# Kernel optimization log

Measured on AMD Instinct MI355X. Metric: run time of the kernel, lower is better.

Reference implementation:

```python
import jax, jax.numpy as jnp
import numpy as np
import math

H = 16
D_MODEL = 1024
D_K = 64
BS = 8
SEQ = 1024


def setup_inputs() -> dict:
    key = jax.random.key(0)
    ks = jax.random.split(key, 13)
    s = 1.0 / math.sqrt(D_MODEL)
    inp = {
        "q": jax.random.normal(ks[0], (BS, SEQ, D_MODEL), dtype=jnp.float32),
        "k": jax.random.normal(ks[1], (BS, SEQ, D_MODEL), dtype=jnp.float32),
        "v": jax.random.normal(ks[2], (BS, SEQ, D_MODEL), dtype=jnp.float32),
        "mask": jax.random.randint(ks[3], (BS, SEQ, SEQ), 0, 2, dtype=jnp.int32),
        "Wq": jax.random.normal(ks[4], (D_MODEL, D_MODEL), dtype=jnp.float32) * s,
        "bq": jax.random.normal(ks[5], (D_MODEL,), dtype=jnp.float32) * s,
        "Wk": jax.random.normal(ks[6], (D_MODEL, D_MODEL), dtype=jnp.float32) * s,
        "bk": jax.random.normal(ks[7], (D_MODEL,), dtype=jnp.float32) * s,
        "Wv": jax.random.normal(ks[8], (D_MODEL, D_MODEL), dtype=jnp.float32) * s,
        "bv": jax.random.normal(ks[9], (D_MODEL,), dtype=jnp.float32) * s,
        "Wo": jax.random.normal(ks[10], (D_MODEL, D_MODEL), dtype=jnp.float32) * s,
        "bo": jax.random.normal(ks[11], (D_MODEL,), dtype=jnp.float32) * s,
    }
    return inp


def reference(q, k, v, mask, Wq, bq, Wk, bk, Wv, bv, Wo, bo):
    bs, seq, _ = q.shape
    # projections, split heads: [b, h, s, dk]
    def proj(x, W, b):
        y = x @ W + b
        return y.reshape(bs, seq, H, D_K).transpose(0, 2, 1, 3)
    qh = proj(q, Wq, bq)
    kh = proj(k, Wk, bk)
    vh = proj(v, Wv, bv)
    # scaled dot-product attention (dropout is identity in eval mode)
    scores = jnp.einsum("bhqd,bhkd->bhqk", qh, kh) / math.sqrt(D_K)
    scores = jnp.where(mask[:, None, :, :] == 0, jnp.float32(-1e9), scores)
    attn = jax.nn.softmax(scores, axis=-1)
    ctx = jnp.einsum("bhqk,bhkd->bhqd", attn, vh)
    concat = ctx.transpose(0, 2, 1, 3).reshape(bs, seq, D_MODEL)
    return concat @ Wo + bo
```

## Files before the change

kernel.cpp:

```cpp
#include <hip/hip_runtime.h>
#include <hip/hip_bf16.h>

#define HN 16
#define DM 1024
#define DK 64
#define BSZ 8
#define SEQL 1024

typedef __attribute__((ext_vector_type(8))) short bf16x8;
typedef __attribute__((ext_vector_type(4))) short short4v;
typedef __attribute__((ext_vector_type(4))) float f32x4;

__device__ __forceinline__ short f2bf(float f) {
    union { float f; unsigned u; } x; x.f = f;
    unsigned u = x.u + 0x7FFFu + ((x.u >> 16) & 1u);
    return (short)(u >> 16);
}

__device__ __forceinline__ void async16(const short* g, short* ldsbase) {
    __builtin_amdgcn_global_load_lds(
        (const __attribute__((address_space(1))) unsigned int*)g,
        (__attribute__((address_space(3))) unsigned int*)ldsbase, 16, 0, 0);
}

__global__ __launch_bounds__(256) void cast_bf16(const float* __restrict__ in,
                                                 short* __restrict__ out) {
    size_t i = (size_t)blockIdx.x * 256 + threadIdx.x;
    float4 a = ((const float4*)in)[2 * i];
    float4 b = ((const float4*)in)[2 * i + 1];
    bf16x8 r = {f2bf(a.x), f2bf(a.y), f2bf(a.z), f2bf(a.w),
                f2bf(b.x), f2bf(b.y), f2bf(b.z), f2bf(b.w)};
    ((bf16x8*)out)[i] = r;
}

__global__ __launch_bounds__(256) void transpose_cast(const float* __restrict__ W,
                                                      short* __restrict__ Wt) {
    __shared__ float tile[32][33];
    const int t = threadIdx.x;
    const int k0 = blockIdx.x * 32, n0 = blockIdx.y * 32;
    const int c = t & 31, r = t >> 5;
    #pragma unroll
    for (int p = 0; p < 4; ++p)
        tile[r + 8 * p][c] = W[(size_t)(k0 + r + 8 * p) * DM + n0 + c];
    __syncthreads();
    #pragma unroll
    for (int p = 0; p < 4; ++p)
        Wt[(size_t)(n0 + r + 8 * p) * DM + k0 + c] = f2bf(tile[c][r + 8 * p]);
}

__global__ __launch_bounds__(256) void pack_mask(const int* __restrict__ mask,
                                                 unsigned long long* __restrict__ bits) {
    size_t i = (size_t)blockIdx.x * 256 + threadIdx.x;
    unsigned long long b = __ballot(mask[i] != 0);
    if ((threadIdx.x & 63) == 0) bits[i >> 6] = b;
}

template <int MODE>
__global__ __launch_bounds__(256) void gemm_mfma(const short* __restrict__ A,
                                                 const short* __restrict__ Wt,
                                                 const float* __restrict__ bias,
                                                 void* __restrict__ Cp) {
    __shared__ __attribute__((aligned(16))) short As[128][32];
    __shared__ __attribute__((aligned(16))) short Bs[128][32];
    const int t = threadIdx.x;
    const int lane = t & 63, wv = t >> 6;
    const int wm = (wv >> 1) * 64, wn = (wv & 1) * 64;
    const int quad = lane >> 4, l15 = lane & 15;
    const int tileM = blockIdx.x * 128, tileN = blockIdx.y * 128;
    const size_t zoff = (size_t)blockIdx.z * DM * SEQL;
    const short* Az = A + zoff;

    const int sr = wv * 16 + (lane >> 2);
    const int sc = (lane & 3) * 8;

    f32x4 acc[4][4];
    #pragma unroll
    for (int i = 0; i < 4; ++i)
        #pragma unroll
        for (int j = 0; j < 4; ++j) acc[i][j] = {0.f, 0.f, 0.f, 0.f};

    for (int k0 = 0; k0 < DM; k0 += 32) {
        #pragma unroll
        for (int p = 0; p < 2; ++p) {
            async16(Az + (size_t)(tileM + p * 64 + sr) * DM + k0 + sc,
                    &As[p * 64 + wv * 16][0]);
            async16(Wt + (size_t)(tileN + p * 64 + sr) * DM + k0 + sc,
                    &Bs[p * 64 + wv * 16][0]);
        }
        __syncthreads();
        bf16x8 a[4], b[4];
        #pragma unroll
        for (int i = 0; i < 4; ++i) a[i] = *(const bf16x8*)&As[wm + i * 16 + l15][quad * 8];
        #pragma unroll
        for (int j = 0; j < 4; ++j) b[j] = *(const bf16x8*)&Bs[wn + j * 16 + l15][quad * 8];
        #pragma unroll
        for (int i = 0; i < 4; ++i)
            #pragma unroll
            for (int j = 0; j < 4; ++j)
                acc[i][j] = __builtin_amdgcn_mfma_f32_16x16x32_bf16(a[i], b[j], acc[i][j], 0, 0, 0);
        __syncthreads();
    }

    #pragma unroll
    for (int i = 0; i < 4; ++i)
        #pragma unroll
        for (int j = 0; j < 4; ++j)
            #pragma unroll
            for (int rr = 0; rr < 4; ++rr) {
                int row = tileM + wm + i * 16 + quad * 4 + rr;
                int col = tileN + wn + j * 16 + l15;
                float v = acc[i][j][rr] + bias[col];
                if (MODE == 0) {
                    short* C = (short*)Cp + zoff;
                    C[((size_t)(col >> 6) * SEQL + row) * DK + (col & 63)] = f2bf(v);
                } else if (MODE == 1) {
                    float* C = (float*)Cp + zoff;
                    C[(size_t)row * DM + col] = v;
                } else {
                    short* C = (short*)Cp + zoff;
                    C[(size_t)col * SEQL + row] = f2bf(v);
                }
            }
}

template <bool USE_BITS>
__global__ __launch_bounds__(256) void attn_mfma(const short* __restrict__ Qw,
                                                 const short* __restrict__ Kw,
                                                 const short* __restrict__ Vt,
                                                 const void* __restrict__ maskp,
                                                 short* __restrict__ ctx) {
    __shared__ __attribute__((aligned(16))) short Qs[64][72];
    __shared__ __attribute__((aligned(16))) short Ks[64][72];
    __shared__ __attribute__((aligned(16))) short Vs[64][72];
    __shared__ __attribute__((aligned(16))) short Ps[4][16][72];
    const int t = threadIdx.x;
    const int lane = t & 63, w = t >> 6;
    const int quad = lane >> 4, l15 = lane & 15;
    const int q0 = blockIdx.x * 64;
    const int h = blockIdx.y;
    const size_t zoff = (size_t)blockIdx.z * DM * SEQL;
    const short* Qb = Qw + zoff + (size_t)h * SEQL * DK;
    const short* Kb = Kw + zoff + (size_t)h * SEQL * DK;
    const short* Vb = Vt + zoff + (size_t)h * DK * SEQL;

    #pragma unroll
    for (int p = 0; p < 2; ++p) {
        int cc = t + 256 * p;
        int row = cc >> 3, off = (cc & 7) * 8;
        *(bf16x8*)&Qs[row][off] = *(const bf16x8*)(Qb + (size_t)(q0 + row) * DK + off);
    }

    f32x4 o[4];
    #pragma unroll
    for (int td = 0; td < 4; ++td) o[td] = {0.f, 0.f, 0.f, 0.f};
    float Lacc[4] = {0.f, 0.f, 0.f, 0.f};

    for (int j0 = 0; j0 < SEQL; j0 += 64) {
        #pragma unroll
        for (int p = 0; p < 2; ++p) {
            int cc = t + 256 * p;
            int row = cc >> 3, off = (cc & 7) * 8;
            *(bf16x8*)&Ks[row][off] = *(const bf16x8*)(Kb + (size_t)(j0 + row) * DK + off);
            *(bf16x8*)&Vs[row][off] = *(const bf16x8*)(Vb + (size_t)row * SEQL + j0 + off);
        }
        __syncthreads();

        unsigned long long mw[4];
        if (USE_BITS) {
            const unsigned long long* mb =
                (const unsigned long long*)maskp + (size_t)blockIdx.z * SEQL * 16;
            #pragma unroll
            for (int rr = 0; rr < 4; ++rr)
                mw[rr] = mb[(size_t)(q0 + w * 16 + quad * 4 + rr) * 16 + (j0 >> 6)];
        }

        #pragma unroll
        for (int tn = 0; tn < 4; ++tn) {
            f32x4 s = {0.f, 0.f, 0.f, 0.f};
            #pragma unroll
            for (int ks = 0; ks < 2; ++ks) {
                bf16x8 aq = *(const bf16x8*)&Qs[w * 16 + l15][ks * 32 + quad * 8];
                bf16x8 bk = *(const bf16x8*)&Ks[tn * 16 + l15][ks * 32 + quad * 8];
                s = __builtin_amdgcn_mfma_f32_16x16x32_bf16(aq, bk, s, 0, 0, 0);
            }
            #pragma unroll
            for (int rr = 0; rr < 4; ++rr) {
                bool keep;
                if (USE_BITS) {
                    keep = (mw[rr] >> (tn * 16 + l15)) & 1ull;
                } else {
                    const int* mb = (const int*)maskp + (size_t)blockIdx.z * SEQL * SEQL;
                    keep = mb[(size_t)(q0 + w * 16 + quad * 4 + rr) * SEQL + j0 + tn * 16 + l15] != 0;
                }
                float p = keep ? __expf(s[rr] * 0.125f) : 0.0f;
                Lacc[rr] += p;
                Ps[w][quad * 4 + rr][tn * 16 + l15] = f2bf(p);
            }
        }
        #pragma unroll
        for (int td = 0; td < 4; ++td)
            #pragma unroll
            for (int ks = 0; ks < 2; ++ks) {
                bf16x8 ap = *(const bf16x8*)&Ps[w][l15][ks * 32 + quad * 8];
                bf16x8 bv = *(const bf16x8*)&Vs[td * 16 + l15][ks * 32 + quad * 8];
                o[td] = __builtin_amdgcn_mfma_f32_16x16x32_bf16(ap, bv, o[td], 0, 0, 0);
            }
        __syncthreads();
    }

    #pragma unroll
    for (int rr = 0; rr < 4; ++rr) {
        float l = Lacc[rr];
        l += __shfl_xor(l, 1);
        l += __shfl_xor(l, 2);
        l += __shfl_xor(l, 4);
        l += __shfl_xor(l, 8);
        Lacc[rr] = 1.0f / l;
    }
    short* cb = ctx + zoff;
    #pragma unroll
    for (int td = 0; td < 4; ++td)
        #pragma unroll
        for (int rr = 0; rr < 4; ++rr) {
            int rq = q0 + w * 16 + quad * 4 + rr;
            int cd = h * 64 + td * 16 + l15;
            cb[(size_t)rq * DM + cd] = f2bf(o[td][rr] * Lacc[rr]);
        }
}

extern "C" void kernel_launch(void* const* d_in, const int* in_sizes, int n_in,
                              void* d_out, int out_size, void* d_ws, size_t ws_size,
                              hipStream_t stream) {
    const float* q  = (const float*)d_in[0];
    const float* k  = (const float*)d_in[1];
    const float* v  = (const float*)d_in[2];
    const int* mask = (const int*)d_in[3];
    const float* Wq = (const float*)d_in[4];
    const float* bq = (const float*)d_in[5];
    const float* Wk = (const float*)d_in[6];
    const float* bk = (const float*)d_in[7];
    const float* Wv = (const float*)d_in[8];
    const float* bv = (const float*)d_in[9];
    const float* Wo = (const float*)d_in[10];
    const float* bo = (const float*)d_in[11];
    float* out = (float*)d_out;

    const size_t MB = (size_t)1 << 20;
    const size_t MEL = (size_t)1024 * 1024;
    char* base = (char*)d_ws;

    short* Wqt = (short*)(base + 0 * 2 * MB);
    short* Wkt = (short*)(base + 1 * 2 * MB);
    short* Wvt = (short*)(base + 2 * 2 * MB);
    short* Wot = (short*)(base + 3 * 2 * MB);

    int zdim;
    bool use_bits;
    if      (ws_size >= 74 * MB) { zdim = 8; use_bits = true; }
    else if (ws_size >= 42 * MB) { zdim = 4; use_bits = true; }
    else if (ws_size >= 26 * MB) { zdim = 2; use_bits = true; }
    else if (ws_size >= 18 * MB) { zdim = 1; use_bits = true; }
    else                         { zdim = 1; use_bits = false; }

    unsigned long long* bits = (unsigned long long*)(base + 8 * MB);
    char* bufs = base + (use_bits ? 9 : 8) * MB;
    const size_t bufB = (size_t)zdim * 2 * MB;
    short* Qw  = (short*)(bufs);
    short* Kw  = (short*)(bufs + bufB);
    short* Vw  = (short*)(bufs + 2 * bufB);
    short* ctx = (short*)(bufs + 3 * bufB);

    transpose_cast<<<dim3(32, 32), 256, 0, stream>>>(Wq, Wqt);
    transpose_cast<<<dim3(32, 32), 256, 0, stream>>>(Wk, Wkt);
    transpose_cast<<<dim3(32, 32), 256, 0, stream>>>(Wv, Wvt);
    transpose_cast<<<dim3(32, 32), 256, 0, stream>>>(Wo, Wot);
    if (use_bits)
        pack_mask<<<(BSZ * SEQL * SEQL) / 256, 256, 0, stream>>>(mask, bits);

    const int iters = BSZ / zdim;
    for (int it = 0; it < iters; ++it) {
        const size_t boff = (size_t)it * zdim * MEL;
        const float* qb = q + boff;
        const float* kb = k + boff;
        const float* vb = v + boff;
        float* ob = out + boff;
        const void* mb = use_bits
            ? (const void*)(bits + (size_t)it * zdim * SEQL * 16)
            : (const void*)(mask + (size_t)it * zdim * SEQL * SEQL);

        const int castGrid = zdim * 512;
        cast_bf16<<<castGrid, 256, 0, stream>>>(qb, ctx);
        gemm_mfma<0><<<dim3(8, 8, zdim), 256, 0, stream>>>(ctx, Wqt, bq, Qw);
        cast_bf16<<<castGrid, 256, 0, stream>>>(kb, ctx);
        gemm_mfma<0><<<dim3(8, 8, zdim), 256, 0, stream>>>(ctx, Wkt, bk, Kw);
        cast_bf16<<<castGrid, 256, 0, stream>>>(vb, ctx);
        gemm_mfma<2><<<dim3(8, 8, zdim), 256, 0, stream>>>(ctx, Wvt, bv, Vw);

        if (use_bits)
            attn_mfma<true><<<dim3(16, 16, zdim), 256, 0, stream>>>(Qw, Kw, Vw, mb, ctx);
        else
            attn_mfma<false><<<dim3(16, 16, zdim), 256, 0, stream>>>(Qw, Kw, Vw, mb, ctx);

        gemm_mfma<1><<<dim3(8, 8, zdim), 256, 0, stream>>>(ctx, Wot, bo, ob);
    }
}
```

Baseline: 408.7 us.

## Transpose score MFMA, vectorize P and V stores, remap attention blocks per XCD

The attention kernel now computes S^T (K as the A operand), so each lane holds four consecutive key columns for one query row. It packs them with v_cvt_pk_bf16_f32 into a single 8-byte LDS store, loads one mask word per lane and reduces the row sum across quads. The V-projection epilogue packs four bf16 values and writes them as one vector store. The attention grid is flattened to 1D and remapped so consecutive blocks of the same head and batch land on the same XCD, improving L2 reuse of K/V at the cost of more index arithmetic and extra shuffles.

```diff
diff --git a/kernel.cpp b/kernel.cpp
--- a/kernel.cpp
+++ b/kernel.cpp
@@ -21,6 +21,15 @@
     __builtin_amdgcn_global_load_lds(
         (const __attribute__((address_space(1))) unsigned int*)g,
         (__attribute__((address_space(3))) unsigned int*)ldsbase, 16, 0, 0);
+}
+
+__device__ __forceinline__ short4v pack4bf(float v0, float v1, float v2, float v3) {
+    unsigned pk0, pk1;
+    asm("v_cvt_pk_bf16_f32 %0, %1, %2" : "=v"(pk0) : "v"(v0), "v"(v1));
+    asm("v_cvt_pk_bf16_f32 %0, %1, %2" : "=v"(pk1) : "v"(v2), "v"(v3));
+    union { unsigned u[2]; short4v s4; } u_;
+    u_.u[0] = pk0; u_.u[1] = pk1;
+    return u_.s4;
 }
 
 __global__ __launch_bounds__(256) void cast_bf16(const float* __restrict__ in,
@@ -101,26 +110,38 @@
         __syncthreads();
     }
 
-    #pragma unroll
-    for (int i = 0; i < 4; ++i)
-        #pragma unroll
-        for (int j = 0; j < 4; ++j)
-            #pragma unroll
-            for (int rr = 0; rr < 4; ++rr) {
-                int row = tileM + wm + i * 16 + quad * 4 + rr;
+    if (MODE == 2) {
+        short* C = (short*)Cp + zoff;
+        #pragma unroll
+        for (int i = 0; i < 4; ++i)
+            #pragma unroll
+            for (int j = 0; j < 4; ++j) {
+                int rowb = tileM + wm + i * 16 + quad * 4;
                 int col = tileN + wn + j * 16 + l15;
-                float v = acc[i][j][rr] + bias[col];
-                if (MODE == 0) {
-                    short* C = (short*)Cp + zoff;
-                    C[((size_t)(col >> 6) * SEQL + row) * DK + (col & 63)] = f2bf(v);
-                } else if (MODE == 1) {
-                    float* C = (float*)Cp + zoff;
-                    C[(size_t)row * DM + col] = v;
-                } else {
-                    short* C = (short*)Cp + zoff;
-                    C[(size_t)col * SEQL + row] = f2bf(v);
+                float b = bias[col];
+                short4v s4 = pack4bf(acc[i][j][0] + b, acc[i][j][1] + b,
+                                     acc[i][j][2] + b, acc[i][j][3] + b);
+                *(short4v*)(C + (size_t)col * SEQL + rowb) = s4;
+            }
+    } else {
+        #pragma unroll
+        for (int i = 0; i < 4; ++i)
+            #pragma unroll
+            for (int j = 0; j < 4; ++j)
+                #pragma unroll
+                for (int rr = 0; rr < 4; ++rr) {
+                    int row = tileM + wm + i * 16 + quad * 4 + rr;
+                    int col = tileN + wn + j * 16 + l15;
+                    float v = acc[i][j][rr] + bias[col];
+                    if (MODE == 0) {
+                        short* C = (short*)Cp + zoff;
+                        C[((size_t)(col >> 6) * SEQL + row) * DK + (col & 63)] = f2bf(v);
+                    } else {
+                        float* C = (float*)Cp + zoff;
+                        C[(size_t)row * DM + col] = v;
+                    }
                 }
-            }
+    }
 }
 
 template <bool USE_BITS>
@@ -136,9 +157,13 @@
     const int t = threadIdx.x;
     const int lane = t & 63, w = t >> 6;
     const int quad = lane >> 4, l15 = lane & 15;
-    const int q0 = blockIdx.x * 64;
-    const int h = blockIdx.y;
-    const size_t zoff = (size_t)blockIdx.z * DM * SEQL;
+    const int nwg = gridDim.x;
+    const int cpx = nwg >> 3;
+    const int vb = (blockIdx.x & 7) * cpx + (blockIdx.x >> 3);
+    const int q0 = (vb & 15) * 64;
+    const int h = (vb >> 4) & 15;
+    const int z = vb >> 8;
+    const size_t zoff = (size_t)z * DM * SEQL;
     const short* Qb = Qw + zoff + (size_t)h * SEQL * DK;
     const short* Kb = Kw + zoff + (size_t)h * SEQL * DK;
     const short* Vb = Vt + zoff + (size_t)h * DK * SEQL;
@@ -153,7 +178,7 @@
     f32x4 o[4];
     #pragma unroll
     for (int td = 0; td < 4; ++td) o[td] = {0.f, 0.f, 0.f, 0.f};
-    float Lacc[4] = {0.f, 0.f, 0.f, 0.f};
+    float Lacc = 0.f;
 
     for (int j0 = 0; j0 < SEQL; j0 += 64) {
         #pragma unroll
@@ -165,13 +190,11 @@
         }
         __syncthreads();
 
-        unsigned long long mw[4];
+        unsigned long long mw = 0;
         if (USE_BITS) {
             const unsigned long long* mb =
-                (const unsigned long long*)maskp + (size_t)blockIdx.z * SEQL * 16;
-            #pragma unroll
-            for (int rr = 0; rr < 4; ++rr)
-                mw[rr] = mb[(size_t)(q0 + w * 16 + quad * 4 + rr) * 16 + (j0 >> 6)];
+                (const unsigned long long*)maskp + (size_t)z * SEQL * 16;
+            mw = mb[(size_t)(q0 + w * 16 + l15) * 16 + (j0 >> 6)];
         }
 
         #pragma unroll
@@ -179,23 +202,26 @@
             f32x4 s = {0.f, 0.f, 0.f, 0.f};
             #pragma unroll
             for (int ks = 0; ks < 2; ++ks) {
-                bf16x8 aq = *(const bf16x8*)&Qs[w * 16 + l15][ks * 32 + quad * 8];
-                bf16x8 bk = *(const bf16x8*)&Ks[tn * 16 + l15][ks * 32 + quad * 8];
-                s = __builtin_amdgcn_mfma_f32_16x16x32_bf16(aq, bk, s, 0, 0, 0);
+                bf16x8 ak = *(const bf16x8*)&Ks[tn * 16 + l15][ks * 32 + quad * 8];
+                bf16x8 bq = *(const bf16x8*)&Qs[w * 16 + l15][ks * 32 + quad * 8];
+                s = __builtin_amdgcn_mfma_f32_16x16x32_bf16(ak, bq, s, 0, 0, 0);
             }
+            float pv[4];
             #pragma unroll
             for (int rr = 0; rr < 4; ++rr) {
                 bool keep;
                 if (USE_BITS) {
-                    keep = (mw[rr] >> (tn * 16 + l15)) & 1ull;
+                    keep = (mw >> (tn * 16 + quad * 4 + rr)) & 1ull;
                 } else {
-                    const int* mb = (const int*)maskp + (size_t)blockIdx.z * SEQL * SEQL;
-                    keep = mb[(size_t)(q0 + w * 16 + quad * 4 + rr) * SEQL + j0 + tn * 16 + l15] != 0;
+                    const int* mi = (const int*)maskp + (size_t)z * SEQL * SEQL;
+                    keep = mi[(size_t)(q0 + w * 16 + l15) * SEQL + j0 + tn * 16 + quad * 4 + rr] != 0;
                 }
-                float p = keep ? __expf(s[rr] * 0.125f) : 0.0f;
-                Lacc[rr] += p;
-                Ps[w][quad * 4 + rr][tn * 16 + l15] = f2bf(p);
+                float e = __expf(s[rr] * 0.125f);
+                pv[rr] = keep ? e : 0.0f;
+                Lacc += pv[rr];
             }
+            *(short4v*)&Ps[w][l15][tn * 16 + quad * 4] =
+                pack4bf(pv[0], pv[1], pv[2], pv[3]);
         }
         #pragma unroll
         for (int td = 0; td < 4; ++td)
@@ -208,15 +234,14 @@
         __syncthreads();
     }
 
-    #pragma unroll
-    for (int rr = 0; rr < 4; ++rr) {
-        float l = Lacc[rr];
-        l += __shfl_xor(l, 1);
-        l += __shfl_xor(l, 2);
-        l += __shfl_xor(l, 4);
-        l += __shfl_xor(l, 8);
-        Lacc[rr] = 1.0f / l;
-    }
+    Lacc += __shfl_xor(Lacc, 16);
+    Lacc += __shfl_xor(Lacc, 32);
+    float Linv = 1.0f / Lacc;
+    float Linv4[4];
+    #pragma unroll
+    for (int rr = 0; rr < 4; ++rr)
+        Linv4[rr] = __shfl(Linv, quad * 4 + rr);
+
     short* cb = ctx + zoff;
     #pragma unroll
     for (int td = 0; td < 4; ++td)
@@ -224,7 +249,7 @@
         for (int rr = 0; rr < 4; ++rr) {
             int rq = q0 + w * 16 + quad * 4 + rr;
             int cd = h * 64 + td * 16 + l15;
-            cb[(size_t)rq * DM + cd] = f2bf(o[td][rr] * Lacc[rr]);
+            cb[(size_t)rq * DM + cd] = f2bf(o[td][rr] * Linv4[rr]);
         }
 }
 
@@ -296,10 +321,11 @@
         cast_bf16<<<castGrid, 256, 0, stream>>>(vb, ctx);
         gemm_mfma<2><<<dim3(8, 8, zdim), 256, 0, stream>>>(ctx, Wvt, bv, Vw);
 
+        const int attnBlocks = 16 * 16 * zdim;
         if (use_bits)
-            attn_mfma<true><<<dim3(16, 16, zdim), 256, 0, stream>>>(Qw, Kw, Vw, mb, ctx);
+            attn_mfma<true><<<attnBlocks, 256, 0, stream>>>(Qw, Kw, Vw, mb, ctx);
         else
-            attn_mfma<false><<<dim3(16, 16, zdim), 256, 0, stream>>>(Qw, Kw, Vw, mb, ctx);
+            attn_mfma<false><<<attnBlocks, 256, 0, stream>>>(Qw, Kw, Vw, mb, ctx);
 
         gemm_mfma<1><<<dim3(8, 8, zdim), 256, 0, stream>>>(ctx, Wot, bo, ob);
     }
```

Result: faster. 396.0 us (-3.1%).
